# Kernel optimization log

Measured on AMD Instinct MI355X. Metric: run time of the kernel, lower is better.

## Reference

```python
import jax, jax.numpy as jnp
import numpy as np

EPS = 1e-7  # keras K.epsilon()
ROUTINGS = 3


def squash(v, axis=-1):
    s = jnp.sum(v * v, axis=axis, keepdims=True)
    scale = s / (1.0 + s) / jnp.sqrt(s + EPS)
    return scale * v


def setup_inputs() -> dict:
    key = jax.random.key(0)
    k1, k2 = jax.random.split(key)
    B, I, K = 256, 2048, 8   # batch, input_num_capsule, input_dim_capsule
    J, D = 10, 16            # num_capsule, dim_capsule
    inputs = jax.random.normal(k1, (B, I, K), dtype=jnp.float32)
    W = jax.random.normal(k2, (J, I, D, K), dtype=jnp.float32) * 0.05
    return {"inputs": inputs, "W": W}


def reference(inputs, W):
    # inputs: [B, I, K]; W: [J, I, D, K]
    # inputs_hat[b,j,i,d] = W[j,i] @ inputs[b,i]  -> [B, J, I, D]
    u_hat = jnp.einsum('jidk,bik->bjid', W, inputs)
    B, J, I, _ = u_hat.shape
    b = jnp.zeros((B, J, 1, I), dtype=u_hat.dtype)
    outputs = None
    for r in range(ROUTINGS):
        c = jax.nn.softmax(b, axis=1)                       # softmax over output capsules
        s = jnp.einsum('bjqi,bjid->bjqd', c, u_hat)          # [B, J, 1, D]
        outputs = squash(s, axis=-1)
        if r < ROUTINGS - 1:
            b = b + jnp.einsum('bjqd,bjid->bjqi', outputs, u_hat)
    return jnp.squeeze(outputs, axis=2)                      # [B, J, D]
```

## Files before the change

kernel.cpp:

```cpp
#include <hip/hip_runtime.h>
#include <math.h>


#define BB 256
#define II 2048
#define KK 8
#define JJ 10
#define DD 16

typedef __attribute__((ext_vector_type(4))) float f32x4;
typedef __attribute__((ext_vector_type(8))) short short8;

__device__ __forceinline__ short f2bf(float f) {
    union { float f; unsigned u; } v; v.f = f;
    unsigned r = v.u + 0x7FFFu + ((v.u >> 16) & 1u);
    return (short)(r >> 16);
}

__global__ __launch_bounds__(256) void cast_w_kernel(const float* __restrict__ W,
                                                     short* __restrict__ Wb) {
    const int idx = blockIdx.x * blockDim.x + threadIdx.x;
    const float4* src = (const float4*)(W + (size_t)idx * 8);
    const float4 a = src[0], b = src[1];
    short8 o;
    o[0] = f2bf(a.x); o[1] = f2bf(a.y); o[2] = f2bf(a.z); o[3] = f2bf(a.w);
    o[4] = f2bf(b.x); o[5] = f2bf(b.y); o[6] = f2bf(b.z); o[7] = f2bf(b.w);
    *(short8*)(Wb + (size_t)idx * 8) = o;
}

__global__ __launch_bounds__(256) void trans_x_kernel(const float* __restrict__ x,
                                                      short* __restrict__ xTb) {
    __shared__ float4 tile[8 * 66];
    const int t = threadIdx.x;
    const int b0 = blockIdx.y * 32, i0 = blockIdx.x * 8;
    {
        const int lb = t >> 3, li = t & 7;
        const float4* src = (const float4*)(x + ((b0 + lb) * II + (i0 + li)) * KK);
        tile[li * 66 + lb * 2 + 0] = src[0];
        tile[li * 66 + lb * 2 + 1] = src[1];
    }
    __syncthreads();
    {
        const int ri = t >> 5, rb = t & 31;
        const float4 p0 = tile[ri * 66 + rb * 2 + 0];
        const float4 p1 = tile[ri * 66 + rb * 2 + 1];
        short8 o;
        o[0] = f2bf(p0.x); o[1] = f2bf(p0.y); o[2] = f2bf(p0.z); o[3] = f2bf(p0.w);
        o[4] = f2bf(p1.x); o[5] = f2bf(p1.y); o[6] = f2bf(p1.z); o[7] = f2bf(p1.w);
        *(short8*)(xTb + ((size_t)(i0 + ri) * BB + (b0 + rb)) * KK) = o;
    }
}

#define LBUF 14336

__device__ __forceinline__ void seg_src_dst(int s, int i0, int b0,
                                            const short* __restrict__ xTb,
                                            const short* __restrict__ Wb,
                                            const short** src, int* dst) {
    if (s < 20) {
        const int j = s >> 1, h = s & 1;
        *src = Wb + ((size_t)(j * II + i0) * DD) * KK + h * 512;
        *dst = j * 1024 + h * 512;
    } else {
        const int il = s - 20;
        *src = xTb + ((size_t)(i0 + il) * BB + b0) * KK;
        *dst = 10240 + il * 512;
    }
}

template <int USE_C>
__global__ __launch_bounds__(256) void round_mfma(
    const short* __restrict__ xTb, const short* __restrict__ Wb,
    const float* __restrict__ vT, float* __restrict__ p)
{
    __shared__ short L[2][LBUF];
    const int t = threadIdx.x;
    const int lane = t & 63, wv = t >> 6;
    const int col = lane & 15, q = lane >> 4;
    const int b0 = blockIdx.y * 64;
    const int bl = wv * 16 + col;
    const int i0 = blockIdx.x * 16;

    short8 r0[7], r1[7];
#pragma unroll
    for (int n = 0; n < 7; ++n) {
        const int s = wv + n * 4;
        const short* src; int dst;
        seg_src_dst(s, i0, b0, xTb, Wb, &src, &dst);
        r0[n] = *(const short8*)(src + lane * 8);
        seg_src_dst(s, i0 + 8, b0, xTb, Wb, &src, &dst);
        r1[n] = *(const short8*)(src + lane * 8);
    }
#pragma unroll
    for (int n = 0; n < 7; ++n) {
        const int s = wv + n * 4;
        const short* src; int dst;
        seg_src_dst(s, i0, b0, xTb, Wb, &src, &dst);
        *(short8*)(&L[0][dst + lane * 8]) = r0[n];
    }
    __syncthreads();

    f32x4 sfrag[JJ];
#pragma unroll
    for (int j = 0; j < JJ; ++j) sfrag[j] = (f32x4){0.f, 0.f, 0.f, 0.f};

    float vfrag[JJ][4];
    if (USE_C) {
#pragma unroll
        for (int j = 0; j < JJ; ++j)
#pragma unroll
            for (int r = 0; r < 4; ++r)
                vfrag[j][r] = vT[(j * DD + q * 4 + r) * BB + b0 + bl];
    }

#pragma unroll
    for (int sc = 0; sc < 2; ++sc) {
        const short* Lb = L[sc];
        if (USE_C) {
            for (int il = 0; il < 8; ++il) {
                short8 A[JJ], Bf;
                const short8 z = (short8){0, 0, 0, 0, 0, 0, 0, 0};
                Bf = z;
#pragma unroll
                for (int j = 0; j < JJ; ++j) A[j] = z;
                if (q == 0) {
                    Bf = *(const short8*)(&Lb[10240 + il * 512 + bl * 8]);
#pragma unroll
                    for (int j = 0; j < JJ; ++j)
                        A[j] = *(const short8*)(&Lb[j * 1024 + il * 128 + col * 8]);
                }
                f32x4 U[JJ];
#pragma unroll
                for (int j = 0; j < JJ; ++j)
                    U[j] = __builtin_amdgcn_mfma_f32_16x16x32_bf16(
                        A[j], Bf, (f32x4){0.f, 0.f, 0.f, 0.f}, 0, 0, 0);
                float Lg[JJ];
#pragma unroll
                for (int j = 0; j < JJ; ++j)
                    Lg[j] = vfrag[j][0] * U[j][0] + vfrag[j][1] * U[j][1]
                          + vfrag[j][2] * U[j][2] + vfrag[j][3] * U[j][3];
#pragma unroll
                for (int j = 0; j < JJ; ++j) {
                    Lg[j] += __shfl_xor(Lg[j], 16, 64);
                    Lg[j] += __shfl_xor(Lg[j], 32, 64);
                }
                float sum = 0.f;
#pragma unroll
                for (int j = 0; j < JJ; ++j) { Lg[j] = __expf(Lg[j]); sum += Lg[j]; }
                const float inv = __builtin_amdgcn_rcpf(sum);
#pragma unroll
                for (int j = 0; j < JJ; ++j) {
                    const float c = Lg[j] * inv;
#pragma unroll
                    for (int r = 0; r < 4; ++r) sfrag[j][r] += c * U[j][r];
                }
            }
        } else {
#pragma unroll
            for (int s = 0; s < 2; ++s) {
                const int il = s * 4 + q;
                const short8 Bf = *(const short8*)(&Lb[10240 + il * 512 + bl * 8]);
#pragma unroll
                for (int j = 0; j < JJ; ++j) {
                    const short8 A = *(const short8*)(&Lb[j * 1024 + il * 128 + col * 8]);
                    sfrag[j] = __builtin_amdgcn_mfma_f32_16x16x32_bf16(A, Bf, sfrag[j], 0, 0, 0);
                }
            }
        }
        if (sc == 0) {
#pragma unroll
            for (int n = 0; n < 7; ++n) {
                const int s = wv + n * 4;
                const short* src; int dst;
                seg_src_dst(s, i0 + 8, b0, xTb, Wb, &src, &dst);
                *(short8*)(&L[1][dst + lane * 8]) = r1[n];
            }
            __syncthreads();
        }
    }

    float* pp = p + ((size_t)(blockIdx.y * 4 + wv) * 128 + blockIdx.x) * (JJ * 256);
#pragma unroll
    for (int j = 0; j < JJ; ++j)
        *(f32x4*)(pp + (j * 64 + lane) * 4) = sfrag[j];
}

template <int MODE>
__global__ __launch_bounds__(256) void rs_kernel(const float* __restrict__ p,
                                                 float* __restrict__ vT,
                                                 float* __restrict__ out, float scale) {
    __shared__ float red[256];
    __shared__ float cf[16];
    const int t = threadIdx.x;
    const int j = blockIdx.x, bt = blockIdx.y;
    const int d = t >> 4, bc = t & 15;
    const int lane = (d >> 2) * 16 + bc, r = d & 3;

    const float* pp = p + (size_t)bt * 128 * (JJ * 256) + j * 256 + lane * 4 + r;
    float sum = 0.f;
#pragma unroll 8
    for (int ch = 0; ch < 128; ++ch) sum += pp[(size_t)ch * (JJ * 256)];
    const float s = sum * scale;

    red[t] = s;
    __syncthreads();
    if (t < 16) {
        float ss = 0.f;
#pragma unroll
        for (int dd = 0; dd < DD; ++dd) {
            const float v = red[dd * 16 + t];
            ss += v * v;
        }
        cf[t] = ss / (1.f + ss) / sqrtf(ss + 1e-7f);
    }
    __syncthreads();
    const float v = cf[bc] * s;
    if (MODE == 0) vT[(j * DD + d) * BB + bt * 16 + bc] = v;
    if (MODE == 1) vT[(j * DD + d) * BB + bt * 16 + bc] += v;
    if (MODE == 2) out[((bt * 16 + bc) * JJ + j) * DD + d] = v;
}

#define IT_OLD 32
#define BT_OLD 16

__global__ __launch_bounds__(256) void zero_kernel(float* __restrict__ p, int n) {
    int idx = blockIdx.x * blockDim.x + threadIdx.x;
    if (idx < n) p[idx] = 0.f;
}

__global__ __launch_bounds__(256) void squash_old(float* __restrict__ s_acc,
                                                  float* __restrict__ dst, float scale,
                                                  int add_to_dst, int zero_src) {
    int idx = blockIdx.x * blockDim.x + threadIdx.x;
    if (idx >= BB * JJ) return;
    float s[DD];
    float ss = 0.f;
#pragma unroll
    for (int d = 0; d < DD; ++d) {
        s[d] = s_acc[idx * DD + d] * scale;
        ss += s[d] * s[d];
    }
    const float coef = ss / (1.f + ss) / sqrtf(ss + 1e-7f);
#pragma unroll
    for (int d = 0; d < DD; ++d) {
        const float vv = coef * s[d];
        if (add_to_dst) dst[idx * DD + d] += vv;
        else            dst[idx * DD + d] = vv;
        if (zero_src)   s_acc[idx * DD + d] = 0.f;
    }
}

__global__ __launch_bounds__(256) void round1_old(const float* __restrict__ x,
                                                  const float* __restrict__ W,
                                                  float* __restrict__ s_acc) {
    const int t = threadIdx.x;
    const int d = t & 15;
    const int bq = t >> 4;
    const int b = blockIdx.y * BT_OLD + bq;
    const int i0 = blockIdx.x * IT_OLD;
    float acc[JJ];
#pragma unroll
    for (int j = 0; j < JJ; ++j) acc[j] = 0.f;
    for (int ii = 0; ii < IT_OLD; ++ii) {
        const int i = i0 + ii;
        const float* xp = x + ((b * II) + i) * KK;
        const float4 xa = *(const float4*)(xp);
        const float4 xb = *(const float4*)(xp + 4);
#pragma unroll
        for (int j = 0; j < JJ; ++j) {
            const float* wp = W + (((j * II + i) * DD + d) * KK);
            const float4 w0 = *(const float4*)(wp);
            const float4 w1 = *(const float4*)(wp + 4);
            acc[j] += w0.x*xa.x + w0.y*xa.y + w0.z*xa.z + w0.w*xa.w
                    + w1.x*xb.x + w1.y*xb.y + w1.z*xb.z + w1.w*xb.w;
        }
    }
#pragma unroll
    for (int j = 0; j < JJ; ++j)
        atomicAdd(&s_acc[(b * JJ + j) * DD + d], acc[j]);
}

__global__ __launch_bounds__(256) void round_old(const float* __restrict__ x,
                                                 const float* __restrict__ W,
                                                 const float* __restrict__ v,
                                                 float* __restrict__ s_acc) {
    const int t = threadIdx.x;
    const int d = t & 15;
    const int bq = t >> 4;
    const int b = blockIdx.y * BT_OLD + bq;
    const int i0 = blockIdx.x * IT_OLD;
    float vr[JJ], acc[JJ];
#pragma unroll
    for (int j = 0; j < JJ; ++j) {
        vr[j] = v[(b * JJ + j) * DD + d];
        acc[j] = 0.f;
    }
    for (int ii = 0; ii < IT_OLD; ++ii) {
        const int i = i0 + ii;
        const float* xp = x + ((b * II) + i) * KK;
        const float4 xa = *(const float4*)(xp);
        const float4 xb = *(const float4*)(xp + 4);
        float U[JJ], Lg[JJ];
#pragma unroll
        for (int j = 0; j < JJ; ++j) {
            const float* wp = W + (((j * II + i) * DD + d) * KK);
            const float4 w0 = *(const float4*)(wp);
            const float4 w1 = *(const float4*)(wp + 4);
            U[j] = w0.x*xa.x + w0.y*xa.y + w0.z*xa.z + w0.w*xa.w
                 + w1.x*xb.x + w1.y*xb.y + w1.z*xb.z + w1.w*xb.w;
            Lg[j] = vr[j] * U[j];
        }
#pragma unroll
        for (int m = 8; m >= 1; m >>= 1) {
#pragma unroll
            for (int j = 0; j < JJ; ++j) Lg[j] += __shfl_xor(Lg[j], m, 64);
        }
        float mx = Lg[0];
#pragma unroll
        for (int j = 1; j < JJ; ++j) mx = fmaxf(mx, Lg[j]);
        float sum = 0.f;
#pragma unroll
        for (int j = 0; j < JJ; ++j) { Lg[j] = __expf(Lg[j] - mx); sum += Lg[j]; }
        const float inv = 1.f / sum;
#pragma unroll
        for (int j = 0; j < JJ; ++j) acc[j] += (Lg[j] * inv) * U[j];
    }
#pragma unroll
    for (int j = 0; j < JJ; ++j)
        atomicAdd(&s_acc[(b * JJ + j) * DD + d], acc[j]);
}

extern "C" void kernel_launch(void* const* d_in, const int* in_sizes, int n_in,
                              void* d_out, int out_size, void* d_ws, size_t ws_size,
                              hipStream_t stream) {
    const float* x = (const float*)d_in[0];
    const float* W = (const float*)d_in[1];
    float* out = (float*)d_out;

    float* vT  = (float*)d_ws;
    float* p   = vT + BB * JJ * DD;
    short* xTb = (short*)(p + (size_t)16 * 128 * 2560);
    short* Wb  = xTb + (size_t)II * BB * KK;
    const size_t need = (size_t)(BB * JJ * DD + 16 * 128 * 2560) * 4
                      + ((size_t)II * BB * KK + (size_t)JJ * II * DD * KK) * 2;

    if (ws_size >= need) {
        cast_w_kernel<<<(JJ * II * DD * KK / 8) / 256, 256, 0, stream>>>(W, Wb);
        trans_x_kernel<<<dim3(II / 8, BB / 32), 256, 0, stream>>>(x, xTb);

        dim3 rg(128, 4);
        dim3 sg(JJ, 16);
        round_mfma<0><<<rg, 256, 0, stream>>>(xTb, Wb, vT, p);
        rs_kernel<0><<<sg, 256, 0, stream>>>(p, vT, out, 0.1f);
        round_mfma<1><<<rg, 256, 0, stream>>>(xTb, Wb, vT, p);
        rs_kernel<1><<<sg, 256, 0, stream>>>(p, vT, out, 1.0f);
        round_mfma<1><<<rg, 256, 0, stream>>>(xTb, Wb, vT, p);
        rs_kernel<2><<<sg, 256, 0, stream>>>(p, vT, out, 1.0f);
    } else {
        float* s_acc = (float*)d_ws;
        float* v_buf = s_acc + BB * JJ * DD;
        const int NS = BB * JJ * DD;
        dim3 rg(II / IT_OLD, BB / BT_OLD);
        zero_kernel<<<(NS + 255) / 256, 256, 0, stream>>>(s_acc, NS);
        round1_old<<<rg, 256, 0, stream>>>(x, W, s_acc);
        squash_old<<<(BB * JJ + 255) / 256, 256, 0, stream>>>(s_acc, v_buf, 0.1f, 0, 1);
        round_old<<<rg, 256, 0, stream>>>(x, W, v_buf, s_acc);
        squash_old<<<(BB * JJ + 255) / 256, 256, 0, stream>>>(s_acc, v_buf, 1.0f, 1, 1);
        round_old<<<rg, 256, 0, stream>>>(x, W, v_buf, s_acc);
        squash_old<<<(BB * JJ + 255) / 256, 256, 0, stream>>>(s_acc, out, 1.0f, 0, 0);
    }
}
```

Before: 162.5 us.

## Fuse routing rounds into persistent kernel with grid barriers and merged prep

Merges the W cast and x transpose into one grid-strided prep kernel. Replaces the six round/reduce launches with one persistent 512-block kernel that uses atomic-counter grid barriers between phases, and falls back to separate launches when occupancy is below 2 blocks per CU. The aim is to remove launch overhead and per-kernel drain/ramp gaps. The cost is spin-wait barrier latency, idle blocks during the reduce phases, and a host-side occupancy query on every call. It also restructures the USE_C inner loop to interleave A loads with the MFMAs.

```diff
diff --git a/kernel.cpp b/kernel.cpp
--- a/kernel.cpp
+++ b/kernel.cpp
@@ -7,6 +7,8 @@
 #define KK 8
 #define JJ 10
 #define DD 16
+#define NCH 128
+#define NBLK 512
 
 typedef __attribute__((ext_vector_type(4))) float f32x4;
 typedef __attribute__((ext_vector_type(8))) short short8;
@@ -17,41 +19,56 @@
     return (short)(r >> 16);
 }
 
-__global__ __launch_bounds__(256) void cast_w_kernel(const float* __restrict__ W,
-                                                     short* __restrict__ Wb) {
-    const int idx = blockIdx.x * blockDim.x + threadIdx.x;
-    const float4* src = (const float4*)(W + (size_t)idx * 8);
-    const float4 a = src[0], b = src[1];
-    short8 o;
-    o[0] = f2bf(a.x); o[1] = f2bf(a.y); o[2] = f2bf(a.z); o[3] = f2bf(a.w);
-    o[4] = f2bf(b.x); o[5] = f2bf(b.y); o[6] = f2bf(b.z); o[7] = f2bf(b.w);
-    *(short8*)(Wb + (size_t)idx * 8) = o;
-}
-
-__global__ __launch_bounds__(256) void trans_x_kernel(const float* __restrict__ x,
-                                                      short* __restrict__ xTb) {
+__global__ __launch_bounds__(256) void prep_kernel(const float* __restrict__ x,
+                                                   const float* __restrict__ W,
+                                                   short* __restrict__ xTb,
+                                                   short* __restrict__ Wb,
+                                                   int* __restrict__ cnt) {
     __shared__ float4 tile[8 * 66];
     const int t = threadIdx.x;
-    const int b0 = blockIdx.y * 32, i0 = blockIdx.x * 8;
-    {
-        const int lb = t >> 3, li = t & 7;
-        const float4* src = (const float4*)(x + ((b0 + lb) * II + (i0 + li)) * KK);
-        tile[li * 66 + lb * 2 + 0] = src[0];
-        tile[li * 66 + lb * 2 + 1] = src[1];
-    }
-    __syncthreads();
-    {
-        const int ri = t >> 5, rb = t & 31;
-        const float4 p0 = tile[ri * 66 + rb * 2 + 0];
-        const float4 p1 = tile[ri * 66 + rb * 2 + 1];
+    if (blockIdx.x == 0 && t < 16) cnt[t] = 0;
+
+    for (int r = blockIdx.x * 256 + t; r < JJ * II * DD; r += NBLK * 256) {
+        const float4* src = (const float4*)(W + (size_t)r * 8);
+        const float4 a = src[0], b = src[1];
         short8 o;
-        o[0] = f2bf(p0.x); o[1] = f2bf(p0.y); o[2] = f2bf(p0.z); o[3] = f2bf(p0.w);
-        o[4] = f2bf(p1.x); o[5] = f2bf(p1.y); o[6] = f2bf(p1.z); o[7] = f2bf(p1.w);
-        *(short8*)(xTb + ((size_t)(i0 + ri) * BB + (b0 + rb)) * KK) = o;
-    }
-}
-
-#define LBUF 14336
+        o[0] = f2bf(a.x); o[1] = f2bf(a.y); o[2] = f2bf(a.z); o[3] = f2bf(a.w);
+        o[4] = f2bf(b.x); o[5] = f2bf(b.y); o[6] = f2bf(b.z); o[7] = f2bf(b.w);
+        *(short8*)(Wb + (size_t)r * 8) = o;
+    }
+
+    for (int tl = blockIdx.x; tl < 2048; tl += NBLK) {
+        const int i0 = (tl & 255) * 8, b0 = (tl >> 8) * 32;
+        __syncthreads();
+        {
+            const int lb = t >> 3, li = t & 7;
+            const float4* src = (const float4*)(x + ((b0 + lb) * II + (i0 + li)) * KK);
+            tile[li * 66 + lb * 2 + 0] = src[0];
+            tile[li * 66 + lb * 2 + 1] = src[1];
+        }
+        __syncthreads();
+        {
+            const int ri = t >> 5, rb = t & 31;
+            const float4 p0 = tile[ri * 66 + rb * 2 + 0];
+            const float4 p1 = tile[ri * 66 + rb * 2 + 1];
+            short8 o;
+            o[0] = f2bf(p0.x); o[1] = f2bf(p0.y); o[2] = f2bf(p0.z); o[3] = f2bf(p0.w);
+            o[4] = f2bf(p1.x); o[5] = f2bf(p1.y); o[6] = f2bf(p1.z); o[7] = f2bf(p1.w);
+            *(short8*)(xTb + ((size_t)(i0 + ri) * BB + (b0 + rb)) * KK) = o;
+        }
+    }
+}
+
+__device__ __forceinline__ void gbar(int* cnt, int phase) {
+    __syncthreads();
+    if (threadIdx.x == 0) {
+        __threadfence();
+        __hip_atomic_fetch_add(&cnt[phase], 1, __ATOMIC_RELEASE, __HIP_MEMORY_SCOPE_AGENT);
+        while (__hip_atomic_load(&cnt[phase], __ATOMIC_ACQUIRE, __HIP_MEMORY_SCOPE_AGENT) < NBLK)
+            __builtin_amdgcn_s_sleep(1);
+    }
+    __syncthreads();
+}
 
 __device__ __forceinline__ void seg_src_dst(int s, int i0, int b0,
                                             const short* __restrict__ xTb,
@@ -69,17 +86,16 @@
 }
 
 template <int USE_C>
-__global__ __launch_bounds__(256) void round_mfma(
+__device__ __forceinline__ void round_body(short (*L)[14336],
     const short* __restrict__ xTb, const short* __restrict__ Wb,
-    const float* __restrict__ vT, float* __restrict__ p)
+    const float* __restrict__ vT, float* __restrict__ p, int chunk, int bgroup)
 {
-    __shared__ short L[2][LBUF];
     const int t = threadIdx.x;
     const int lane = t & 63, wv = t >> 6;
     const int col = lane & 15, q = lane >> 4;
-    const int b0 = blockIdx.y * 64;
+    const int b0 = bgroup * 64;
     const int bl = wv * 16 + col;
-    const int i0 = blockIdx.x * 16;
+    const int i0 = chunk * 16;
 
     short8 r0[7], r1[7];
 #pragma unroll
@@ -118,27 +134,20 @@
         const short* Lb = L[sc];
         if (USE_C) {
             for (int il = 0; il < 8; ++il) {
-                short8 A[JJ], Bf;
                 const short8 z = (short8){0, 0, 0, 0, 0, 0, 0, 0};
-                Bf = z;
-#pragma unroll
-                for (int j = 0; j < JJ; ++j) A[j] = z;
-                if (q == 0) {
-                    Bf = *(const short8*)(&Lb[10240 + il * 512 + bl * 8]);
-#pragma unroll
-                    for (int j = 0; j < JJ; ++j)
-                        A[j] = *(const short8*)(&Lb[j * 1024 + il * 128 + col * 8]);
-                }
+                short8 Bf = z;
+                if (q == 0) Bf = *(const short8*)(&Lb[10240 + il * 512 + bl * 8]);
                 f32x4 U[JJ];
-#pragma unroll
-                for (int j = 0; j < JJ; ++j)
+                float Lg[JJ];
+#pragma unroll
+                for (int j = 0; j < JJ; ++j) {
+                    short8 Aj = z;
+                    if (q == 0) Aj = *(const short8*)(&Lb[j * 1024 + il * 128 + col * 8]);
                     U[j] = __builtin_amdgcn_mfma_f32_16x16x32_bf16(
-                        A[j], Bf, (f32x4){0.f, 0.f, 0.f, 0.f}, 0, 0, 0);
-                float Lg[JJ];
-#pragma unroll
-                for (int j = 0; j < JJ; ++j)
+                        Aj, Bf, (f32x4){0.f, 0.f, 0.f, 0.f}, 0, 0, 0);
                     Lg[j] = vfrag[j][0] * U[j][0] + vfrag[j][1] * U[j][1]
                           + vfrag[j][2] * U[j][2] + vfrag[j][3] * U[j][3];
+                }
 #pragma unroll
                 for (int j = 0; j < JJ; ++j) {
                     Lg[j] += __shfl_xor(Lg[j], 16, 64);
@@ -157,13 +166,13 @@
             }
         } else {
 #pragma unroll
-            for (int s = 0; s < 2; ++s) {
-                const int il = s * 4 + q;
+            for (int g = 0; g < 2; ++g) {
+                const int il = g * 4 + q;
                 const short8 Bf = *(const short8*)(&Lb[10240 + il * 512 + bl * 8]);
 #pragma unroll
                 for (int j = 0; j < JJ; ++j) {
-                    const short8 A = *(const short8*)(&Lb[j * 1024 + il * 128 + col * 8]);
-                    sfrag[j] = __builtin_amdgcn_mfma_f32_16x16x32_bf16(A, Bf, sfrag[j], 0, 0, 0);
+                    const short8 Aj = *(const short8*)(&Lb[j * 1024 + il * 128 + col * 8]);
+                    sfrag[j] = __builtin_amdgcn_mfma_f32_16x16x32_bf16(Aj, Bf, sfrag[j], 0, 0, 0);
                 }
             }
         }
@@ -179,27 +188,25 @@
         }
     }
 
-    float* pp = p + ((size_t)(blockIdx.y * 4 + wv) * 128 + blockIdx.x) * (JJ * 256);
+    float* pp = p + ((size_t)(bgroup * 4 + wv) * NCH + chunk) * (JJ * 256);
 #pragma unroll
     for (int j = 0; j < JJ; ++j)
         *(f32x4*)(pp + (j * 64 + lane) * 4) = sfrag[j];
 }
 
 template <int MODE>
-__global__ __launch_bounds__(256) void rs_kernel(const float* __restrict__ p,
-                                                 float* __restrict__ vT,
-                                                 float* __restrict__ out, float scale) {
-    __shared__ float red[256];
-    __shared__ float cf[16];
+__device__ __forceinline__ void rs_body(float* red, float* cf,
+    const float* __restrict__ p, float* __restrict__ vT, float* __restrict__ out,
+    float scale, int j, int bt)
+{
     const int t = threadIdx.x;
-    const int j = blockIdx.x, bt = blockIdx.y;
     const int d = t >> 4, bc = t & 15;
     const int lane = (d >> 2) * 16 + bc, r = d & 3;
 
-    const float* pp = p + (size_t)bt * 128 * (JJ * 256) + j * 256 + lane * 4 + r;
+    const float* pp = p + (size_t)bt * NCH * (JJ * 256) + j * 256 + lane * 4 + r;
     float sum = 0.f;
 #pragma unroll 8
-    for (int ch = 0; ch < 128; ++ch) sum += pp[(size_t)ch * (JJ * 256)];
+    for (int ch = 0; ch < NCH; ++ch) sum += pp[(size_t)ch * (JJ * 256)];
     const float s = sum * scale;
 
     red[t] = s;
@@ -220,114 +227,46 @@
     if (MODE == 2) out[((bt * 16 + bc) * JJ + j) * DD + d] = v;
 }
 
-#define IT_OLD 32
-#define BT_OLD 16
-
-__global__ __launch_bounds__(256) void zero_kernel(float* __restrict__ p, int n) {
-    int idx = blockIdx.x * blockDim.x + threadIdx.x;
-    if (idx < n) p[idx] = 0.f;
-}
-
-__global__ __launch_bounds__(256) void squash_old(float* __restrict__ s_acc,
-                                                  float* __restrict__ dst, float scale,
-                                                  int add_to_dst, int zero_src) {
-    int idx = blockIdx.x * blockDim.x + threadIdx.x;
-    if (idx >= BB * JJ) return;
-    float s[DD];
-    float ss = 0.f;
-#pragma unroll
-    for (int d = 0; d < DD; ++d) {
-        s[d] = s_acc[idx * DD + d] * scale;
-        ss += s[d] * s[d];
-    }
-    const float coef = ss / (1.f + ss) / sqrtf(ss + 1e-7f);
-#pragma unroll
-    for (int d = 0; d < DD; ++d) {
-        const float vv = coef * s[d];
-        if (add_to_dst) dst[idx * DD + d] += vv;
-        else            dst[idx * DD + d] = vv;
-        if (zero_src)   s_acc[idx * DD + d] = 0.f;
-    }
-}
-
-__global__ __launch_bounds__(256) void round1_old(const float* __restrict__ x,
-                                                  const float* __restrict__ W,
-                                                  float* __restrict__ s_acc) {
-    const int t = threadIdx.x;
-    const int d = t & 15;
-    const int bq = t >> 4;
-    const int b = blockIdx.y * BT_OLD + bq;
-    const int i0 = blockIdx.x * IT_OLD;
-    float acc[JJ];
-#pragma unroll
-    for (int j = 0; j < JJ; ++j) acc[j] = 0.f;
-    for (int ii = 0; ii < IT_OLD; ++ii) {
-        const int i = i0 + ii;
-        const float* xp = x + ((b * II) + i) * KK;
-        const float4 xa = *(const float4*)(xp);
-        const float4 xb = *(const float4*)(xp + 4);
-#pragma unroll
-        for (int j = 0; j < JJ; ++j) {
-            const float* wp = W + (((j * II + i) * DD + d) * KK);
-            const float4 w0 = *(const float4*)(wp);
-            const float4 w1 = *(const float4*)(wp + 4);
-            acc[j] += w0.x*xa.x + w0.y*xa.y + w0.z*xa.z + w0.w*xa.w
-                    + w1.x*xb.x + w1.y*xb.y + w1.z*xb.z + w1.w*xb.w;
-        }
-    }
-#pragma unroll
-    for (int j = 0; j < JJ; ++j)
-        atomicAdd(&s_acc[(b * JJ + j) * DD + d], acc[j]);
-}
-
-__global__ __launch_bounds__(256) void round_old(const float* __restrict__ x,
-                                                 const float* __restrict__ W,
-                                                 const float* __restrict__ v,
-                                                 float* __restrict__ s_acc) {
-    const int t = threadIdx.x;
-    const int d = t & 15;
-    const int bq = t >> 4;
-    const int b = blockIdx.y * BT_OLD + bq;
-    const int i0 = blockIdx.x * IT_OLD;
-    float vr[JJ], acc[JJ];
-#pragma unroll
-    for (int j = 0; j < JJ; ++j) {
-        vr[j] = v[(b * JJ + j) * DD + d];
-        acc[j] = 0.f;
-    }
-    for (int ii = 0; ii < IT_OLD; ++ii) {
-        const int i = i0 + ii;
-        const float* xp = x + ((b * II) + i) * KK;
-        const float4 xa = *(const float4*)(xp);
-        const float4 xb = *(const float4*)(xp + 4);
-        float U[JJ], Lg[JJ];
-#pragma unroll
-        for (int j = 0; j < JJ; ++j) {
-            const float* wp = W + (((j * II + i) * DD + d) * KK);
-            const float4 w0 = *(const float4*)(wp);
-            const float4 w1 = *(const float4*)(wp + 4);
-            U[j] = w0.x*xa.x + w0.y*xa.y + w0.z*xa.z + w0.w*xa.w
-                 + w1.x*xb.x + w1.y*xb.y + w1.z*xb.z + w1.w*xb.w;
-            Lg[j] = vr[j] * U[j];
-        }
-#pragma unroll
-        for (int m = 8; m >= 1; m >>= 1) {
-#pragma unroll
-            for (int j = 0; j < JJ; ++j) Lg[j] += __shfl_xor(Lg[j], m, 64);
-        }
-        float mx = Lg[0];
-#pragma unroll
-        for (int j = 1; j < JJ; ++j) mx = fmaxf(mx, Lg[j]);
-        float sum = 0.f;
-#pragma unroll
-        for (int j = 0; j < JJ; ++j) { Lg[j] = __expf(Lg[j] - mx); sum += Lg[j]; }
-        const float inv = 1.f / sum;
-#pragma unroll
-        for (int j = 0; j < JJ; ++j) acc[j] += (Lg[j] * inv) * U[j];
-    }
-#pragma unroll
-    for (int j = 0; j < JJ; ++j)
-        atomicAdd(&s_acc[(b * JJ + j) * DD + d], acc[j]);
+__global__ __launch_bounds__(256, 2) void caps_kernel(
+    const short* __restrict__ xTb, const short* __restrict__ Wb,
+    float* __restrict__ vT, float* __restrict__ p, float* __restrict__ out,
+    int* __restrict__ cnt)
+{
+    __shared__ short Ls[2][14336];
+    float* red = (float*)&Ls[0][0];
+    float* cf  = red + 256;
+    const int bid = blockIdx.x;
+    const int chunk = bid & (NCH - 1), bgroup = bid >> 7;
+    const int rj = bid >> 4, rbt = bid & 15;
+
+    round_body<0>(Ls, xTb, Wb, vT, p, chunk, bgroup);
+    gbar(cnt, 0);
+    if (bid < JJ * 16) rs_body<0>(red, cf, p, vT, out, 0.1f, rj, rbt);
+    gbar(cnt, 1);
+    round_body<1>(Ls, xTb, Wb, vT, p, chunk, bgroup);
+    gbar(cnt, 2);
+    if (bid < JJ * 16) rs_body<1>(red, cf, p, vT, out, 1.0f, rj, rbt);
+    gbar(cnt, 3);
+    round_body<1>(Ls, xTb, Wb, vT, p, chunk, bgroup);
+    gbar(cnt, 4);
+    if (bid < JJ * 16) rs_body<2>(red, cf, p, vT, out, 1.0f, rj, rbt);
+}
+
+template <int USE_C>
+__global__ __launch_bounds__(256) void round_mfma_k(const short* __restrict__ xTb,
+                                                    const short* __restrict__ Wb,
+                                                    const float* __restrict__ vT,
+                                                    float* __restrict__ p) {
+    __shared__ short Ls[2][14336];
+    round_body<USE_C>(Ls, xTb, Wb, vT, p, blockIdx.x, blockIdx.y);
+}
+
+template <int MODE>
+__global__ __launch_bounds__(256) void rs_k(const float* __restrict__ p,
+                                            float* __restrict__ vT,
+                                            float* __restrict__ out, float scale) {
+    __shared__ float red[256 + 16];
+    rs_body<MODE>(red, red + 256, p, vT, out, scale, blockIdx.x, blockIdx.y);
 }
 
 extern "C" void kernel_launch(void* const* d_in, const int* in_sizes, int n_in,
@@ -337,36 +276,27 @@
     const float* W = (const float*)d_in[1];
     float* out = (float*)d_out;
 
-    float* vT  = (float*)d_ws;
+    int*   cnt = (int*)d_ws;
+    float* vT  = (float*)d_ws + 64;
     float* p   = vT + BB * JJ * DD;
-    short* xTb = (short*)(p + (size_t)16 * 128 * 2560);
+    short* xTb = (short*)(p + (size_t)16 * NCH * 2560);
     short* Wb  = xTb + (size_t)II * BB * KK;
-    const size_t need = (size_t)(BB * JJ * DD + 16 * 128 * 2560) * 4
-                      + ((size_t)II * BB * KK + (size_t)JJ * II * DD * KK) * 2;
-
-    if (ws_size >= need) {
-        cast_w_kernel<<<(JJ * II * DD * KK / 8) / 256, 256, 0, stream>>>(W, Wb);
-        trans_x_kernel<<<dim3(II / 8, BB / 32), 256, 0, stream>>>(x, xTb);
-
-        dim3 rg(128, 4);
+
+    int occ = 0;
+    hipError_t oe = hipOccupancyMaxActiveBlocksPerMultiprocessor(&occ, caps_kernel, 256, 0);
+
+    prep_kernel<<<NBLK, 256, 0, stream>>>(x, W, xTb, Wb, cnt);
+
+    if (oe == hipSuccess && occ >= 2) {
+        caps_kernel<<<NBLK, 256, 0, stream>>>(xTb, Wb, vT, p, out, cnt);
+    } else {
+        dim3 rg(NCH, 4);
         dim3 sg(JJ, 16);
-        round_mfma<0><<<rg, 256, 0, stream>>>(xTb, Wb, vT, p);
-        rs_kernel<0><<<sg, 256, 0, stream>>>(p, vT, out, 0.1f);
-        round_mfma<1><<<rg, 256, 0, stream>>>(xTb, Wb, vT, p);
-        rs_kernel<1><<<sg, 256, 0, stream>>>(p, vT, out, 1.0f);
-        round_mfma<1><<<rg, 256, 0, stream>>>(xTb, Wb, vT, p);
-        rs_kernel<2><<<sg, 256, 0, stream>>>(p, vT, out, 1.0f);
-    } else {
-        float* s_acc = (float*)d_ws;
-        float* v_buf = s_acc + BB * JJ * DD;
-        const int NS = BB * JJ * DD;
-        dim3 rg(II / IT_OLD, BB / BT_OLD);
-        zero_kernel<<<(NS + 255) / 256, 256, 0, stream>>>(s_acc, NS);
-        round1_old<<<rg, 256, 0, stream>>>(x, W, s_acc);
-        squash_old<<<(BB * JJ + 255) / 256, 256, 0, stream>>>(s_acc, v_buf, 0.1f, 0, 1);
-        round_old<<<rg, 256, 0, stream>>>(x, W, v_buf, s_acc);
-        squash_old<<<(BB * JJ + 255) / 256, 256, 0, stream>>>(s_acc, v_buf, 1.0f, 1, 1);
-        round_old<<<rg, 256, 0, stream>>>(x, W, v_buf, s_acc);
-        squash_old<<<(BB * JJ + 255) / 256, 256, 0, stream>>>(s_acc, out, 1.0f, 0, 0);
-    }
-}
+        round_mfma_k<0><<<rg, 256, 0, stream>>>(xTb, Wb, vT, p);
+        rs_k<0><<<sg, 256, 0, stream>>>(p, vT, out, 0.1f);
+        round_mfma_k<1><<<rg, 256, 0, stream>>>(xTb, Wb, vT, p);
+        rs_k<1><<<sg, 256, 0, stream>>>(p, vT, out, 1.0f);
+        round_mfma_k<1><<<rg, 256, 0, stream>>>(xTb, Wb, vT, p);
+        rs_k<2><<<sg, 256, 0, stream>>>(p, vT, out, 1.0f);
+    }
+}
```

Measured after the change: 163.3 us. No clear change (+0.5%).

## Split routing round into two MFMA passes with LDS-staged softmax coefficients

Applied to the files above, without the earlier changes.

The weighted routing round no longer keeps all ten u_hat fragments live in registers. It computes logits in a first MFMA pass, stores them in the idle half of the LDS double buffer, and runs the softmax there spread across all lanes. A second MFMA pass then recomputes u_hat and accumulates with the stored coefficients. Separately, the W cast and x transpose kernels are merged into one grid-stride prep kernel to save a launch. The cost is twice the MFMA and LDS traffic plus an extra barrier, in exchange for lower register pressure and more parallel softmax work.

```diff
diff --git a/kernel.cpp b/kernel.cpp
--- a/kernel.cpp
+++ b/kernel.cpp
@@ -7,6 +7,8 @@
 #define KK 8
 #define JJ 10
 #define DD 16
+#define NCH 128
+#define LGS (8 * JJ * 17)
 
 typedef __attribute__((ext_vector_type(4))) float f32x4;
 typedef __attribute__((ext_vector_type(8))) short short8;
@@ -17,41 +19,43 @@
     return (short)(r >> 16);
 }
 
-__global__ __launch_bounds__(256) void cast_w_kernel(const float* __restrict__ W,
-                                                     short* __restrict__ Wb) {
-    const int idx = blockIdx.x * blockDim.x + threadIdx.x;
-    const float4* src = (const float4*)(W + (size_t)idx * 8);
-    const float4 a = src[0], b = src[1];
-    short8 o;
-    o[0] = f2bf(a.x); o[1] = f2bf(a.y); o[2] = f2bf(a.z); o[3] = f2bf(a.w);
-    o[4] = f2bf(b.x); o[5] = f2bf(b.y); o[6] = f2bf(b.z); o[7] = f2bf(b.w);
-    *(short8*)(Wb + (size_t)idx * 8) = o;
-}
-
-__global__ __launch_bounds__(256) void trans_x_kernel(const float* __restrict__ x,
-                                                      short* __restrict__ xTb) {
+__global__ __launch_bounds__(256) void prep_kernel(const float* __restrict__ x,
+                                                   const float* __restrict__ W,
+                                                   short* __restrict__ xTb,
+                                                   short* __restrict__ Wb) {
     __shared__ float4 tile[8 * 66];
     const int t = threadIdx.x;
-    const int b0 = blockIdx.y * 32, i0 = blockIdx.x * 8;
-    {
-        const int lb = t >> 3, li = t & 7;
-        const float4* src = (const float4*)(x + ((b0 + lb) * II + (i0 + li)) * KK);
-        tile[li * 66 + lb * 2 + 0] = src[0];
-        tile[li * 66 + lb * 2 + 1] = src[1];
-    }
-    __syncthreads();
-    {
-        const int ri = t >> 5, rb = t & 31;
-        const float4 p0 = tile[ri * 66 + rb * 2 + 0];
-        const float4 p1 = tile[ri * 66 + rb * 2 + 1];
+
+    for (int r = blockIdx.x * 256 + t; r < JJ * II * DD; r += 512 * 256) {
+        const float4* src = (const float4*)(W + (size_t)r * 8);
+        const float4 a = src[0], b = src[1];
         short8 o;
-        o[0] = f2bf(p0.x); o[1] = f2bf(p0.y); o[2] = f2bf(p0.z); o[3] = f2bf(p0.w);
-        o[4] = f2bf(p1.x); o[5] = f2bf(p1.y); o[6] = f2bf(p1.z); o[7] = f2bf(p1.w);
-        *(short8*)(xTb + ((size_t)(i0 + ri) * BB + (b0 + rb)) * KK) = o;
-    }
-}
-
-#define LBUF 14336
+        o[0] = f2bf(a.x); o[1] = f2bf(a.y); o[2] = f2bf(a.z); o[3] = f2bf(a.w);
+        o[4] = f2bf(b.x); o[5] = f2bf(b.y); o[6] = f2bf(b.z); o[7] = f2bf(b.w);
+        *(short8*)(Wb + (size_t)r * 8) = o;
+    }
+
+    for (int tl = blockIdx.x; tl < 2048; tl += 512) {
+        const int i0 = (tl & 255) * 8, b0 = (tl >> 8) * 32;
+        __syncthreads();
+        {
+            const int lb = t >> 3, li = t & 7;
+            const float4* src = (const float4*)(x + ((b0 + lb) * II + (i0 + li)) * KK);
+            tile[li * 66 + lb * 2 + 0] = src[0];
+            tile[li * 66 + lb * 2 + 1] = src[1];
+        }
+        __syncthreads();
+        {
+            const int ri = t >> 5, rb = t & 31;
+            const float4 p0 = tile[ri * 66 + rb * 2 + 0];
+            const float4 p1 = tile[ri * 66 + rb * 2 + 1];
+            short8 o;
+            o[0] = f2bf(p0.x); o[1] = f2bf(p0.y); o[2] = f2bf(p0.z); o[3] = f2bf(p0.w);
+            o[4] = f2bf(p1.x); o[5] = f2bf(p1.y); o[6] = f2bf(p1.z); o[7] = f2bf(p1.w);
+            *(short8*)(xTb + ((size_t)(i0 + ri) * BB + (b0 + rb)) * KK) = o;
+        }
+    }
+}
 
 __device__ __forceinline__ void seg_src_dst(int s, int i0, int b0,
                                             const short* __restrict__ xTb,
@@ -69,17 +73,16 @@
 }
 
 template <int USE_C>
-__global__ __launch_bounds__(256) void round_mfma(
+__device__ __forceinline__ void round_body(short (*L)[14336],
     const short* __restrict__ xTb, const short* __restrict__ Wb,
-    const float* __restrict__ vT, float* __restrict__ p)
+    const float* __restrict__ vT, float* __restrict__ p, int chunk, int bgroup)
 {
-    __shared__ short L[2][LBUF];
     const int t = threadIdx.x;
     const int lane = t & 63, wv = t >> 6;
     const int col = lane & 15, q = lane >> 4;
-    const int b0 = blockIdx.y * 64;
+    const int b0 = bgroup * 64;
     const int bl = wv * 16 + col;
-    const int i0 = blockIdx.x * 16;
+    const int i0 = chunk * 16;
 
     short8 r0[7], r1[7];
 #pragma unroll
@@ -117,57 +120,79 @@
     for (int sc = 0; sc < 2; ++sc) {
         const short* Lb = L[sc];
         if (USE_C) {
+            float* lgw = (float*)(&L[1 - sc][0]) + wv * LGS;
+            const short8 z = (short8){0, 0, 0, 0, 0, 0, 0, 0};
+
             for (int il = 0; il < 8; ++il) {
-                short8 A[JJ], Bf;
-                const short8 z = (short8){0, 0, 0, 0, 0, 0, 0, 0};
-                Bf = z;
-#pragma unroll
-                for (int j = 0; j < JJ; ++j) A[j] = z;
-                if (q == 0) {
-                    Bf = *(const short8*)(&Lb[10240 + il * 512 + bl * 8]);
-#pragma unroll
-                    for (int j = 0; j < JJ; ++j)
-                        A[j] = *(const short8*)(&Lb[j * 1024 + il * 128 + col * 8]);
-                }
-                f32x4 U[JJ];
-#pragma unroll
-                for (int j = 0; j < JJ; ++j)
-                    U[j] = __builtin_amdgcn_mfma_f32_16x16x32_bf16(
-                        A[j], Bf, (f32x4){0.f, 0.f, 0.f, 0.f}, 0, 0, 0);
+                short8 Bf = z;
+                if (q == 0) Bf = *(const short8*)(&Lb[10240 + il * 512 + bl * 8]);
                 float Lg[JJ];
 #pragma unroll
-                for (int j = 0; j < JJ; ++j)
-                    Lg[j] = vfrag[j][0] * U[j][0] + vfrag[j][1] * U[j][1]
-                          + vfrag[j][2] * U[j][2] + vfrag[j][3] * U[j][3];
+                for (int j = 0; j < JJ; ++j) {
+                    short8 Aj = z;
+                    if (q == 0) Aj = *(const short8*)(&Lb[j * 1024 + il * 128 + col * 8]);
+                    const f32x4 U = __builtin_amdgcn_mfma_f32_16x16x32_bf16(
+                        Aj, Bf, (f32x4){0.f, 0.f, 0.f, 0.f}, 0, 0, 0);
+                    Lg[j] = vfrag[j][0] * U[0] + vfrag[j][1] * U[1]
+                          + vfrag[j][2] * U[2] + vfrag[j][3] * U[3];
+                }
 #pragma unroll
                 for (int j = 0; j < JJ; ++j) {
                     Lg[j] += __shfl_xor(Lg[j], 16, 64);
                     Lg[j] += __shfl_xor(Lg[j], 32, 64);
                 }
+                if (q == 0) {
+#pragma unroll
+                    for (int j = 0; j < JJ; ++j)
+                        lgw[(il * JJ + j) * 17 + col] = Lg[j];
+                }
+            }
+
+#pragma unroll
+            for (int pp = 0; pp < 2; ++pp) {
+                const int pr = pp * 64 + lane;
+                const int ib = pr >> 4, bb = pr & 15;
+                float e[JJ];
                 float sum = 0.f;
 #pragma unroll
-                for (int j = 0; j < JJ; ++j) { Lg[j] = __expf(Lg[j]); sum += Lg[j]; }
+                for (int j = 0; j < JJ; ++j) {
+                    e[j] = __expf(lgw[(ib * JJ + j) * 17 + bb]);
+                    sum += e[j];
+                }
                 const float inv = __builtin_amdgcn_rcpf(sum);
 #pragma unroll
+                for (int j = 0; j < JJ; ++j)
+                    lgw[(ib * JJ + j) * 17 + bb] = e[j] * inv;
+            }
+
+            for (int il = 0; il < 8; ++il) {
+                short8 Bf = z;
+                if (q == 0) Bf = *(const short8*)(&Lb[10240 + il * 512 + bl * 8]);
+#pragma unroll
                 for (int j = 0; j < JJ; ++j) {
-                    const float c = Lg[j] * inv;
-#pragma unroll
-                    for (int r = 0; r < 4; ++r) sfrag[j][r] += c * U[j][r];
+                    short8 Aj = z;
+                    if (q == 0) Aj = *(const short8*)(&Lb[j * 1024 + il * 128 + col * 8]);
+                    const f32x4 U = __builtin_amdgcn_mfma_f32_16x16x32_bf16(
+                        Aj, Bf, (f32x4){0.f, 0.f, 0.f, 0.f}, 0, 0, 0);
+                    const float c = lgw[(il * JJ + j) * 17 + col];
+#pragma unroll
+                    for (int r = 0; r < 4; ++r) sfrag[j][r] += c * U[r];
                 }
             }
         } else {
 #pragma unroll
-            for (int s = 0; s < 2; ++s) {
-                const int il = s * 4 + q;
+            for (int g = 0; g < 2; ++g) {
+                const int il = g * 4 + q;
                 const short8 Bf = *(const short8*)(&Lb[10240 + il * 512 + bl * 8]);
 #pragma unroll
                 for (int j = 0; j < JJ; ++j) {
-                    const short8 A = *(const short8*)(&Lb[j * 1024 + il * 128 + col * 8]);
-                    sfrag[j] = __builtin_amdgcn_mfma_f32_16x16x32_bf16(A, Bf, sfrag[j], 0, 0, 0);
+                    const short8 Aj = *(const short8*)(&Lb[j * 1024 + il * 128 + col * 8]);
+                    sfrag[j] = __builtin_amdgcn_mfma_f32_16x16x32_bf16(Aj, Bf, sfrag[j], 0, 0, 0);
                 }
             }
         }
         if (sc == 0) {
+            if (USE_C) __syncthreads();
 #pragma unroll
             for (int n = 0; n < 7; ++n) {
                 const int s = wv + n * 4;
@@ -179,16 +204,25 @@
         }
     }
 
-    float* pp = p + ((size_t)(blockIdx.y * 4 + wv) * 128 + blockIdx.x) * (JJ * 256);
+    float* pp = p + ((size_t)(bgroup * 4 + wv) * NCH + chunk) * (JJ * 256);
 #pragma unroll
     for (int j = 0; j < JJ; ++j)
         *(f32x4*)(pp + (j * 64 + lane) * 4) = sfrag[j];
 }
 
+template <int USE_C>
+__global__ __launch_bounds__(256) void round_mfma_k(const short* __restrict__ xTb,
+                                                    const short* __restrict__ Wb,
+                                                    const float* __restrict__ vT,
+                                                    float* __restrict__ p) {
+    __shared__ short Ls[2][14336];
+    round_body<USE_C>(Ls, xTb, Wb, vT, p, blockIdx.x, blockIdx.y);
+}
+
 template <int MODE>
-__global__ __launch_bounds__(256) void rs_kernel(const float* __restrict__ p,
-                                                 float* __restrict__ vT,
-                                                 float* __restrict__ out, float scale) {
+__global__ __launch_bounds__(256) void rs_k(const float* __restrict__ p,
+                                            float* __restrict__ vT,
+                                            float* __restrict__ out, float scale) {
     __shared__ float red[256];
     __shared__ float cf[16];
     const int t = threadIdx.x;
@@ -196,10 +230,10 @@
     const int d = t >> 4, bc = t & 15;
     const int lane = (d >> 2) * 16 + bc, r = d & 3;
 
-    const float* pp = p + (size_t)bt * 128 * (JJ * 256) + j * 256 + lane * 4 + r;
+    const float* pp = p + (size_t)bt * NCH * (JJ * 256) + j * 256 + lane * 4 + r;
     float sum = 0.f;
 #pragma unroll 8
-    for (int ch = 0; ch < 128; ++ch) sum += pp[(size_t)ch * (JJ * 256)];
+    for (int ch = 0; ch < NCH; ++ch) sum += pp[(size_t)ch * (JJ * 256)];
     const float s = sum * scale;
 
     red[t] = s;
@@ -339,23 +373,22 @@
 
     float* vT  = (float*)d_ws;
     float* p   = vT + BB * JJ * DD;
-    short* xTb = (short*)(p + (size_t)16 * 128 * 2560);
+    short* xTb = (short*)(p + (size_t)16 * NCH * 2560);
     short* Wb  = xTb + (size_t)II * BB * KK;
-    const size_t need = (size_t)(BB * JJ * DD + 16 * 128 * 2560) * 4
+    const size_t need = (size_t)(BB * JJ * DD + 16 * NCH * 2560) * 4
                       + ((size_t)II * BB * KK + (size_t)JJ * II * DD * KK) * 2;
 
     if (ws_size >= need) {
-        cast_w_kernel<<<(JJ * II * DD * KK / 8) / 256, 256, 0, stream>>>(W, Wb);
-        trans_x_kernel<<<dim3(II / 8, BB / 32), 256, 0, stream>>>(x, xTb);
-
-        dim3 rg(128, 4);
+        prep_kernel<<<512, 256, 0, stream>>>(x, W, xTb, Wb);
+
+        dim3 rg(NCH, 4);
         dim3 sg(JJ, 16);
-        round_mfma<0><<<rg, 256, 0, stream>>>(xTb, Wb, vT, p);
-        rs_kernel<0><<<sg, 256, 0, stream>>>(p, vT, out, 0.1f);
-        round_mfma<1><<<rg, 256, 0, stream>>>(xTb, Wb, vT, p);
-        rs_kernel<1><<<sg, 256, 0, stream>>>(p, vT, out, 1.0f);
-        round_mfma<1><<<rg, 256, 0, stream>>>(xTb, Wb, vT, p);
-        rs_kernel<2><<<sg, 256, 0, stream>>>(p, vT, out, 1.0f);
+        round_mfma_k<0><<<rg, 256, 0, stream>>>(xTb, Wb, vT, p);
+        rs_k<0><<<sg, 256, 0, stream>>>(p, vT, out, 0.1f);
+        round_mfma_k<1><<<rg, 256, 0, stream>>>(xTb, Wb, vT, p);
+        rs_k<1><<<sg, 256, 0, stream>>>(p, vT, out, 1.0f);
+        round_mfma_k<1><<<rg, 256, 0, stream>>>(xTb, Wb, vT, p);
+        rs_k<2><<<sg, 256, 0, stream>>>(p, vT, out, 1.0f);
     } else {
         float* s_acc = (float*)d_ws;
         float* v_buf = s_acc + BB * JJ * DD;
```

New measurement: 475.3 us. 193% more time.
